# Optimization experiments

Measured on AMD Instinct MI355X. Metric: run time of the kernel, lower is better.

Reference implementation:

```python
import jax, jax.numpy as jnp
from jax import lax
import numpy as np

B, T, D_IN, H, EPS = 32, 256, 256, 1024, 1e-5


def setup_inputs() -> dict:
    key = jax.random.key(0)
    ks = jax.random.split(key, 9)
    s = lambda fan_in: 1.0 / np.sqrt(fan_in)
    merged0, merged1 = D_IN + H, H + H
    series = jax.random.normal(ks[0], (B, T, D_IN), dtype=jnp.float32)
    # Fused gate weights: columns are [in_gate | forget | candidate | out] (4 Linears concatenated)
    W0 = jax.random.uniform(ks[1], (merged0, 4 * H), jnp.float32, -s(merged0), s(merged0))
    b0 = jax.random.uniform(ks[2], (4 * H,), jnp.float32, -s(merged0), s(merged0))
    g0 = jnp.ones((H,), jnp.float32)
    beta0 = jnp.zeros((H,), jnp.float32)
    W1 = jax.random.uniform(ks[3], (merged1, 4 * H), jnp.float32, -s(merged1), s(merged1))
    b1 = jax.random.uniform(ks[4], (4 * H,), jnp.float32, -s(merged1), s(merged1))
    g1 = jnp.ones((H,), jnp.float32)
    beta1 = jnp.zeros((H,), jnp.float32)
    return {"series": series, "W0": W0, "b0": b0, "g0": g0, "beta0": beta0,
            "W1": W1, "b1": b1, "g1": g1, "beta1": beta1}


def _layer_norm(x, g, beta):
    mu = jnp.mean(x, axis=-1, keepdims=True)
    var = jnp.mean((x - mu) ** 2, axis=-1, keepdims=True)
    return (x - mu) * lax.rsqrt(var + EPS) * g + beta


def _run_layer(x_seq, W, b, g, beta):
    # x_seq: [B, T, D]; exp-gated LSTM cell scanned over time
    batch = x_seq.shape[0]

    def step(carry, x_t):
        h, c = carry
        merged = jnp.concatenate([x_t, h], axis=-1)          # [B, D+H]
        z = merged @ W + b                                    # [B, 4H] fused 4 projections
        zi, zf, zc, zo = jnp.split(z, 4, axis=-1)
        in_gate = jnp.exp(jnp.clip(zi, -6.0, 3.0))
        forget_gate = jnp.exp(jnp.clip(zf, -6.0, 3.0))
        candidate = jnp.tanh(zc)
        c_next = forget_gate * c + in_gate * candidate
        h_next = jax.nn.sigmoid(zo) * jnp.tanh(_layer_norm(c_next, g, beta))
        return (h_next, c_next), h_next

    h0 = jnp.zeros((batch, H), x_seq.dtype)
    c0 = jnp.zeros((batch, H), x_seq.dtype)
    _, hs = lax.scan(step, (h0, c0), jnp.swapaxes(x_seq, 0, 1))  # hs: [T, B, H]
    return jnp.swapaxes(hs, 0, 1)


def reference(series, W0, b0, g0, beta0, W1, b1, g1, beta1):
    out = _run_layer(series, W0, b0, g0, beta0)
    # dropout p=0.0 -> identity between layers
    out = _run_layer(out, W1, b1, g1, beta1)
    return out[:, -1, :]
```

## Files before the change

### kernel.cpp

```cpp
#include <hip/hip_runtime.h>
#include <hip/hip_bf16.h>
#include <cstddef>

typedef __bf16 bf16_t;
typedef _Float16 f16_t;
typedef bf16_t bf16x8 __attribute__((ext_vector_type(8)));
typedef bf16_t bf16x4 __attribute__((ext_vector_type(4)));
typedef f16_t  f16x8  __attribute__((ext_vector_type(8)));
typedef float  f32x4  __attribute__((ext_vector_type(4)));
typedef unsigned u32x4 __attribute__((ext_vector_type(4)));
typedef unsigned u32x2 __attribute__((ext_vector_type(2)));

#define T_STEPS 256
#define BATCH   32
#define HDIM    1024
#define ZDIM    4096

constexpr size_t SZ_HSEQ  = (size_t)8192 * 1024 * 2;
constexpr size_t SZ_HBUF  = (size_t)2 * 32 * 512 * 4;
constexpr size_t SZ_SP    = (size_t)2 * 4 * 8 * 128 * 4;
constexpr size_t SZ_HST   = (size_t)32 * 1024 * 2;
constexpr size_t SZ_CST   = (size_t)32 * 1024 * 4;
constexpr size_t SZ_MU    = 256;
constexpr size_t SZ_TAIL  = SZ_HBUF + SZ_SP + 2*SZ_HST + SZ_CST + SZ_MU;
constexpr int    FILL_WORDS = (int)((SZ_HBUF + SZ_SP) / 4);

constexpr int SLAB_STRIDE = 264;
constexpr int HL_STRIDE   = 1040;
constexpr int SCAN_LDS    = 2 * 64 * SLAB_STRIDE * 2;

__global__ void init_fill(unsigned* __restrict__ p, int n) {
    int i = blockIdx.x * blockDim.x + threadIdx.x;
    if (i < n) p[i] = 0xFFFFFFFFu;
}

__device__ __forceinline__ void split_bf16(float v, bf16_t& hi, bf16_t& lo) {
    hi = (bf16_t)v;
    lo = (bf16_t)(v - (float)hi);
}
__device__ __forceinline__ unsigned short f16_bits(f16_t f) {
    union { unsigned short u; f16_t f2; } x; x.f2 = f; return x.u;
}
__device__ __forceinline__ float tanh_fast(float x) {
    float e = __expf(2.f * x);
    return 1.f - 2.f * __builtin_amdgcn_rcpf(e + 1.f);
}
__device__ __forceinline__ void bar_lds() {
    asm volatile("s_waitcnt lgkmcnt(0)" ::: "memory");
    __builtin_amdgcn_s_barrier();
    asm volatile("" ::: "memory");
}

template<int KTOT, int MODE>
__global__ __launch_bounds__(256) void gemm_xp(
    const float*  __restrict__ Afp,
    const bf16_t* __restrict__ Ahi,
    const bf16_t* __restrict__ Alo,
    const float*  __restrict__ W,
    const float*  __restrict__ bias,
    float*        __restrict__ xp,
    int t0)
{
    __shared__ bf16_t Ash[64][40], Asl[64][40], Bsh[64][40], Bsl[64][40];
    const int bm = blockIdx.x / (ZDIM/64);
    const int bn = blockIdx.x % (ZDIM/64);
    const int tid  = threadIdx.x;
    const int lane = tid & 63;
    const int w    = tid >> 6;
    const int wm = w >> 1, wn = w & 1;
    const int q   = lane >> 4;
    const int l15 = lane & 15;

    f32x4 acc[2][2] = {};

    const int sm = tid & 63;
    const int sk = (tid >> 6) * 8;
    const int gr = t0*32 + bm*64 + sm;
    const float*  Arow  = nullptr;
    const bf16_t* Ahrow = nullptr;
    const bf16_t* Alrow = nullptr;
    if constexpr (MODE == 0) {
        int tt = gr >> 5, bb = gr & 31;
        Arow = Afp + ((size_t)bb * T_STEPS + tt) * 256;
    } else {
        Ahrow = Ahi + (size_t)gr * HDIM;
        Alrow = Alo + (size_t)gr * HDIM;
    }
    const int gcol = bn*64 + sm;

    for (int k0 = 0; k0 < KTOT; k0 += 32) {
        if constexpr (MODE == 0) {
            f32x4 a0 = *(const f32x4*)(Arow + k0 + sk);
            f32x4 a1 = *(const f32x4*)(Arow + k0 + sk + 4);
            #pragma unroll
            for (int j = 0; j < 4; ++j) {
                split_bf16(a0[j], Ash[sm][sk+j],   Asl[sm][sk+j]);
                split_bf16(a1[j], Ash[sm][sk+4+j], Asl[sm][sk+4+j]);
            }
        } else {
            *(bf16x8*)&Ash[sm][sk] = *(const bf16x8*)(Ahrow + k0 + sk);
            *(bf16x8*)&Asl[sm][sk] = *(const bf16x8*)(Alrow + k0 + sk);
        }
        #pragma unroll
        for (int j = 0; j < 8; ++j) {
            float wv = W[(size_t)(k0 + sk + j) * ZDIM + gcol];
            split_bf16(wv, Bsh[sm][sk+j], Bsl[sm][sk+j]);
        }
        __syncthreads();
        #pragma unroll
        for (int mt = 0; mt < 2; ++mt) {
            #pragma unroll
            for (int nt = 0; nt < 2; ++nt) {
                bf16x8 ah = *(const bf16x8*)&Ash[wm*32 + mt*16 + l15][q*8];
                bf16x8 al = *(const bf16x8*)&Asl[wm*32 + mt*16 + l15][q*8];
                bf16x8 bh = *(const bf16x8*)&Bsh[wn*32 + nt*16 + l15][q*8];
                bf16x8 bl = *(const bf16x8*)&Bsl[wn*32 + nt*16 + l15][q*8];
                acc[mt][nt] = __builtin_amdgcn_mfma_f32_16x16x32_bf16(ah, bh, acc[mt][nt], 0, 0, 0);
                acc[mt][nt] = __builtin_amdgcn_mfma_f32_16x16x32_bf16(al, bh, acc[mt][nt], 0, 0, 0);
                acc[mt][nt] = __builtin_amdgcn_mfma_f32_16x16x32_bf16(ah, bl, acc[mt][nt], 0, 0, 0);
            }
        }
        __syncthreads();
    }
    #pragma unroll
    for (int mt = 0; mt < 2; ++mt) {
        int row = bm*64 + wm*32 + mt*16 + q*4;
        #pragma unroll
        for (int nt = 0; nt < 2; ++nt) {
            int col = bn*64 + wn*32 + nt*16 + l15;
            float bia = bias[col];
            #pragma unroll
            for (int r = 0; r < 4; ++r)
                xp[(size_t)(row + r)*ZDIM + col] = acc[mt][nt][r] + bia;
        }
    }
}

__global__ __launch_bounds__(256, 1) void scan_kernel(
    const float* __restrict__ Wh,
    const float* __restrict__ xp,
    const float* __restrict__ gamma,
    const float* __restrict__ beta,
    unsigned*    Hbuf,
    unsigned*    Sp,
    bf16_t*      __restrict__ hseq_hi,
    bf16_t*      __restrict__ hseq_lo,
    float*       __restrict__ outlast,
    bf16_t*      __restrict__ hst_hi,
    bf16_t*      __restrict__ hst_lo,
    float*       __restrict__ cstate,
    float*       __restrict__ mustate,
    int t0, int t1)
{
    extern __shared__ char smem[];
    f16_t* slab_hi = (f16_t*)smem;
    f16_t* slab_lo = (f16_t*)(smem + 64*SLAB_STRIDE*2);
    f16_t* hl      = (f16_t*)smem;
    float* swred   = (float*)(smem + 8*HL_STRIDE*2);
    float* sredS   = swred + 64;

    const int gid = blockIdx.x >> 6;
    const int lid = blockIdx.x & 63;
    const int B0  = gid * 8;
    const int H0  = lid * 16;
    const int tid  = threadIdx.x;
    const int lane = tid & 63;
    const int w    = tid >> 6;
    const int q    = lane >> 4;
    const int l15  = lane & 15;

    f16x8 wf_hi[32], wf_lo[32];
    {
        const int kw   = tid >> 6;
        const int strip= (tid >> 4) & 3;
        const int col  = tid & 15;
        const int gc2  = strip*1024 + H0 + col;
        const int rr_w = col*4 + strip;
        #pragma unroll
        for (int s = 0; s < 4; ++s) {
            for (int j = 0; j < 64; ++j) {
                int kk = j*4 + kw;
                float v = Wh[(size_t)(s*256 + kk)*ZDIM + gc2];
                f16_t hi = (f16_t)v;
                f16_t lo = (f16_t)((v - (float)hi) * 2048.f);
                slab_hi[rr_w*SLAB_STRIDE + kk] = hi;
                slab_lo[rr_w*SLAB_STRIDE + kk] = lo;
            }
            __syncthreads();
            #pragma unroll
            for (int kbl = 0; kbl < 8; ++kbl) {
                wf_hi[s*8+kbl] = *(const f16x8*)&slab_hi[(16*w + l15)*SLAB_STRIDE + kbl*32 + q*8];
                wf_lo[s*8+kbl] = *(const f16x8*)&slab_lo[(16*w + l15)*SLAB_STRIDE + kbl*32 + q*8];
            }
            __syncthreads();
        }
    }

    const int  bidx  = l15;
    const bool valid = bidx < 8;
    const int  batch = B0 + bidx;
    const int  hcl   = 4*w + q;
    const int  hcg   = H0 + hcl;
    const size_t xpbase = (size_t)batch * ZDIM + (size_t)H0 + hcl;
    const int hrow  = (l15 < 8) ? l15 : 7;

    const int half   = lane >> 5;
    const int lane32 = lane & 31;
    const int rr     = 2*w + half;
    const int rbatch = B0 + rr;

    float g_own = 0.f, b_own = 0.f;
    if (valid) { g_own = gamma[hcg]; b_own = beta[hcg]; }

    float c = 0.f, mu_own = 0.f;
    if (t0 > 0) {
        if (valid) {
            c = cstate[(size_t)batch*HDIM + hcg];
            mu_own = mustate[batch];
        }
        const int cb = tid * 4;
        #pragma unroll
        for (int r = 0; r < 8; ++r) {
            bf16x4 vh = *(const bf16x4*)&hst_hi[(size_t)(B0+r)*HDIM + cb];
            bf16x4 vl = *(const bf16x4*)&hst_lo[(size_t)(B0+r)*HDIM + cb];
            #pragma unroll
            for (int e = 0; e < 4; ++e)
                hl[r*HL_STRIDE + cb + e] = (f16_t)((float)vh[e] + (float)vl[e]);
        }
    }
    __syncthreads();

    float xpv[4] = {0.f, 0.f, 0.f, 0.f};
    if (valid) {
        const float* xpt = xp + xpbase;
        #pragma unroll
        for (int r = 0; r < 4; ++r) xpv[r] = xpt[(size_t)r * 1024];
    }

    const bool is_l0 = (hseq_hi != nullptr);

    #pragma unroll 1
    for (int t = t0; t < t1; ++t) {
        f32x4 acc_hh = {0.f,0.f,0.f,0.f}, acc_lh = acc_hh;
        if (t > 0) {
            const f16_t* Bp = hl + (size_t)hrow * HL_STRIDE + q*8;
            #pragma unroll
            for (int kb = 0; kb < 32; ++kb) {
                f16x8 b = *(const f16x8*)(Bp + kb*32);
                acc_hh = __builtin_amdgcn_mfma_f32_16x16x32_f16(wf_hi[kb], b, acc_hh, 0, 0, 0);
                acc_lh = __builtin_amdgcn_mfma_f32_16x16x32_f16(wf_lo[kb], b, acc_lh, 0, 0, 0);
            }
        }
        float z[4];
        #pragma unroll
        for (int r = 0; r < 4; ++r)
            z[r] = (acc_hh[r] + acc_lh[r]*(1.f/2048.f)) + xpv[r];

        float zi = fminf(fmaxf(z[0], -6.f), 3.f);
        float zf = fminf(fmaxf(z[1], -6.f), 3.f);
        float ig = __expf(zi);
        float fg = __expf(zf);
        float cand = tanh_fast(z[2]);
        float sg = 1.f / (1.f + __expf(-z[3]));
        c = fg * c + ig * cand;

        const int par = t & 1;
        const unsigned tg = (unsigned)(t & 3);
        const unsigned tgpat = (unsigned)(t & 1) | (((unsigned)(t >> 1) & 1u) << 16);

        float dm = valid ? (c - mu_own) : 0.f;
        float s1 = dm, s2 = dm*dm;
        s1 += __shfl_xor(s1, 16); s2 += __shfl_xor(s2, 16);
        s1 += __shfl_xor(s1, 32); s2 += __shfl_xor(s2, 32);
        if (lane < 8) { swred[(w*8+lane)*2] = s1; swred[(w*8+lane)*2+1] = s2; }
        bar_lds();

        if (tid < 8) {
            float S1p = swred[tid*2]       + swred[(8+tid)*2]
                      + swred[(16+tid)*2]  + swred[(24+tid)*2];
            float S2p = swred[tid*2+1]     + swred[(8+tid)*2+1]
                      + swred[(16+tid)*2+1]+ swred[(24+tid)*2+1];
            u32x2 pk;
            pk[0] = (__float_as_uint(S1p) & ~3u) | tg;
            pk[1] = (__float_as_uint(S2p) & ~3u) | tg;
            *(volatile u32x2*)(Sp + (((size_t)par*4 + gid)*8 + tid)*128 + (size_t)lid*2) = pk;
        }

        if (valid && t+1 < t1) {
            const float* xpt = xp + (size_t)(t+1 - t0) * (BATCH*ZDIM) + xpbase;
            #pragma unroll
            for (int r = 0; r < 4; ++r) xpv[r] = xpt[(size_t)r * 1024];
        }

        {
            const int prr = tid >> 5, jj = tid & 31;
            volatile const u32x4* spb =
                (volatile const u32x4*)(Sp + (((size_t)par*4 + gid)*8 + prr)*128 + (size_t)jj*4);
            u32x4 sv = *spb;
            while ((((sv[0]^tg)|(sv[1]^tg)|(sv[2]^tg)|(sv[3]^tg)) & 3u) != 0u) {
                __builtin_amdgcn_s_sleep(1);
                sv = *spb;
            }
            float s1p = __uint_as_float(sv[0] & ~3u) + __uint_as_float(sv[2] & ~3u);
            float s2p = __uint_as_float(sv[1] & ~3u) + __uint_as_float(sv[3] & ~3u);
            #pragma unroll
            for (int m = 1; m < 32; m <<= 1) {
                s1p += __shfl_xor(s1p, m);
                s2p += __shfl_xor(s2p, m);
            }
            if (jj == 0) { sredS[prr*2] = s1p; sredS[prr*2+1] = s2p; }
        }
        bar_lds();

        const bool carry = (t == t1-1) && (t1 < T_STEPS);
        unsigned hbs = 0;
        if (valid) {
            float S1 = sredS[bidx*2], S2 = sredS[bidx*2+1];
            float dmu = S1 * (1.f/1024.f);
            float mu  = mu_own + dmu;
            float var = S2 * (1.f/1024.f) - dmu*dmu;
            float rsig = rsqrtf(var + 1e-5f);
            mu_own = mu;
            float ln   = (c - mu) * rsig * g_own + b_own;
            float hval = sg * tanh_fast(ln);
            if (is_l0) {
                bf16_t hi, lo; split_bf16(hval, hi, lo);
                hseq_hi[((size_t)t*32 + batch)*HDIM + hcg] = hi;
                hseq_lo[((size_t)t*32 + batch)*HDIM + hcg] = lo;
            }
            if (carry) {
                bf16_t hi, lo; split_bf16(hval, hi, lo);
                hst_hi[(size_t)batch*HDIM + hcg] = hi;
                hst_lo[(size_t)batch*HDIM + hcg] = lo;
            }
            if (outlast && t == T_STEPS-1)
                outlast[(size_t)batch*HDIM + hcg] = hval;
            unsigned tb = (q & 1) ? ((unsigned)(t >> 1) & 1u) : ((unsigned)t & 1u);
            hbs = ((unsigned)f16_bits((f16_t)hval) & 0xFFFEu) | tb;
        }
        unsigned pb2 = __shfl_xor(hbs, 16);
        if (valid && !(q & 1)) {
            unsigned dw = hbs | (pb2 << 16);
            *(volatile unsigned*)(Hbuf + ((size_t)par*32 + batch)*512 + ((unsigned)hcg >> 1)) = dw;
        }

        volatile const u32x4* hb4 =
            (volatile const u32x4*)(Hbuf + ((size_t)par*32 + rbatch)*512) + lane32;
        u32x4 pv[4];
        #pragma unroll
        for (int k = 0; k < 4; ++k) pv[k] = hb4[(size_t)k*32];
        for (;;) {
            bool bad = false;
            #pragma unroll
            for (int k = 0; k < 4; ++k) {
                unsigned m = ((pv[k][0]^tgpat)|(pv[k][1]^tgpat)
                             |(pv[k][2]^tgpat)|(pv[k][3]^tgpat)) & 0x00010001u;
                if (m) { pv[k] = hb4[(size_t)k*32]; bad = true; }
            }
            if (!bad) break;
            __builtin_amdgcn_s_sleep(1);
        }
        #pragma unroll
        for (int k = 0; k < 4; ++k) {
            u32x4 vv = pv[k] & 0xFFFEFFFEu;
            *(u32x4*)&hl[(size_t)rr*HL_STRIDE + (size_t)k*256 + (size_t)lane32*8] = vv;
        }
        bar_lds();
    }

    if (t1 < T_STEPS) {
        if (valid) cstate[(size_t)batch*HDIM + hcg] = c;
        if (lid == 0 && w == 0 && q == 0 && valid) mustate[batch] = mu_own;
    }
}

extern "C" void kernel_launch(void* const* d_in, const int* in_sizes, int n_in,
                              void* d_out, int out_size, void* d_ws, size_t ws_size,
                              hipStream_t stream) {
    (void)in_sizes; (void)n_in;
    const float* series = (const float*)d_in[0];
    const float* W0  = (const float*)d_in[1];
    const float* b0  = (const float*)d_in[2];
    const float* g0  = (const float*)d_in[3];
    const float* be0 = (const float*)d_in[4];
    const float* W1  = (const float*)d_in[5];
    const float* b1  = (const float*)d_in[6];
    const float* g1  = (const float*)d_in[7];
    const float* be1 = (const float*)d_in[8];
    float* out = (float*)d_out;
    unsigned char* ws = (unsigned char*)d_ws;

    int cT = 0;
    const int cands[4] = {256, 128, 64, 32};
    for (int i = 0; i < 4; ++i) {
        size_t need = (size_t)cands[i]*32*ZDIM*4 + 2*SZ_HSEQ + SZ_TAIL;
        if (need <= ws_size) { cT = cands[i]; break; }
    }
    if (cT == 0) {
        (void)hipMemsetAsync(d_out, 0, (size_t)out_size * sizeof(float), stream);
        return;
    }
    const size_t sz_xp = (size_t)cT*32*ZDIM*4;
    unsigned char* p = ws;
    float*    xp      = (float*)p;    p += sz_xp;
    bf16_t*   hseq_hi = (bf16_t*)p;   p += SZ_HSEQ;
    bf16_t*   hseq_lo = (bf16_t*)p;   p += SZ_HSEQ;
    unsigned* Hbuf    = (unsigned*)p; p += SZ_HBUF;
    unsigned* Sp      = (unsigned*)p; p += SZ_SP;
    bf16_t*   hst_hi  = (bf16_t*)p;   p += SZ_HST;
    bf16_t*   hst_lo  = (bf16_t*)p;   p += SZ_HST;
    float*    cstate  = (float*)p;    p += SZ_CST;
    float*    mustate = (float*)p;

    (void)hipFuncSetAttribute((const void*)scan_kernel,
                              hipFuncAttributeMaxDynamicSharedMemorySize, SCAN_LDS);

    const int nch = T_STEPS / cT;
    const int gemm_grid = (cT*32/64) * (ZDIM/64);

    init_fill<<<(FILL_WORDS + 255)/256, 256, 0, stream>>>(Hbuf, FILL_WORDS);
    for (int ci = 0; ci < nch; ++ci) {
        int t0 = ci*cT, t1 = t0 + cT;
        gemm_xp<256, 0><<<gemm_grid, 256, 0, stream>>>(
            series, nullptr, nullptr, W0, b0, xp, t0);
        scan_kernel<<<256, 256, SCAN_LDS, stream>>>(
            W0 + (size_t)256*ZDIM, xp, g0, be0, Hbuf, Sp,
            hseq_hi, hseq_lo, nullptr, hst_hi, hst_lo, cstate, mustate, t0, t1);
    }
    init_fill<<<(FILL_WORDS + 255)/256, 256, 0, stream>>>(Hbuf, FILL_WORDS);
    for (int ci = 0; ci < nch; ++ci) {
        int t0 = ci*cT, t1 = t0 + cT;
        gemm_xp<1024, 1><<<gemm_grid, 256, 0, stream>>>(
            nullptr, hseq_hi, hseq_lo, W1, b1, xp, t0);
        scan_kernel<<<256, 256, SCAN_LDS, stream>>>(
            W1 + (size_t)1024*ZDIM, xp, g1, be1, Hbuf, Sp,
            nullptr, nullptr, out, hst_hi, hst_lo, cstate, mustate, t0, t1);
    }
}
```

Baseline: 4.172 ms.

## Merge two scan blocks per workgroup to halve cross-block sync participants

The persistent scan kernel now runs 128 workgroups of 512 threads, each holding two 16-column hidden slices, instead of 256 workgroups of 256 threads. This halves the number of partial layer-norm sums exchanged through global memory and the number of blocks in each spin-wait, and each block now loads only 8 batch rows of h per step. The final step's h exchange is also skipped. The cost is a longer serialized weight preload, more LDS reduction work per block, and fewer blocks spread across the CUs.

```diff
diff --git a/kernel.cpp b/kernel.cpp
--- a/kernel.cpp
+++ b/kernel.cpp
@@ -18,7 +18,7 @@
 
 constexpr size_t SZ_HSEQ  = (size_t)8192 * 1024 * 2;
 constexpr size_t SZ_HBUF  = (size_t)2 * 32 * 512 * 4;
-constexpr size_t SZ_SP    = (size_t)2 * 4 * 8 * 128 * 4;
+constexpr size_t SZ_SP    = (size_t)2 * 4 * 8 * 32 * 8;
 constexpr size_t SZ_HST   = (size_t)32 * 1024 * 2;
 constexpr size_t SZ_CST   = (size_t)32 * 1024 * 4;
 constexpr size_t SZ_MU    = 256;
@@ -136,7 +136,7 @@
     }
 }
 
-__global__ __launch_bounds__(256, 1) void scan_kernel(
+__global__ __launch_bounds__(512, 1) void scan_kernel(
     const float* __restrict__ Wh,
     const float* __restrict__ xp,
     const float* __restrict__ gamma,
@@ -157,57 +157,63 @@
     f16_t* slab_lo = (f16_t*)(smem + 64*SLAB_STRIDE*2);
     f16_t* hl      = (f16_t*)smem;
     float* swred   = (float*)(smem + 8*HL_STRIDE*2);
-    float* sredS   = swred + 64;
-
-    const int gid = blockIdx.x >> 6;
-    const int lid = blockIdx.x & 63;
+    float* sredS   = swred + 128;
+
+    const int gid = blockIdx.x >> 5;
+    const int sub = blockIdx.x & 31;
     const int B0  = gid * 8;
-    const int H0  = lid * 16;
     const int tid  = threadIdx.x;
     const int lane = tid & 63;
     const int w    = tid >> 6;
+    const int wl   = w & 3;
+    const int vb   = w >> 2;
+    const int vlid = sub*2 + vb;
+    const int H0   = vlid * 16;
     const int q    = lane >> 4;
     const int l15  = lane & 15;
 
     f16x8 wf_hi[32], wf_lo[32];
     {
-        const int kw   = tid >> 6;
+        const int col  = tid & 15;
         const int strip= (tid >> 4) & 3;
-        const int col  = tid & 15;
-        const int gc2  = strip*1024 + H0 + col;
+        const int kw   = (tid >> 6) & 3;
+        const int rep  = tid >> 8;
         const int rr_w = col*4 + strip;
-        #pragma unroll
-        for (int s = 0; s < 4; ++s) {
-            for (int j = 0; j < 64; ++j) {
-                int kk = j*4 + kw;
-                float v = Wh[(size_t)(s*256 + kk)*ZDIM + gc2];
-                f16_t hi = (f16_t)v;
-                f16_t lo = (f16_t)((v - (float)hi) * 2048.f);
-                slab_hi[rr_w*SLAB_STRIDE + kk] = hi;
-                slab_lo[rr_w*SLAB_STRIDE + kk] = lo;
-            }
-            __syncthreads();
-            #pragma unroll
-            for (int kbl = 0; kbl < 8; ++kbl) {
-                wf_hi[s*8+kbl] = *(const f16x8*)&slab_hi[(16*w + l15)*SLAB_STRIDE + kbl*32 + q*8];
-                wf_lo[s*8+kbl] = *(const f16x8*)&slab_lo[(16*w + l15)*SLAB_STRIDE + kbl*32 + q*8];
-            }
-            __syncthreads();
+        for (int p = 0; p < 2; ++p) {
+            const int gc2 = strip*1024 + (sub*2 + p)*16 + col;
+            #pragma unroll 1
+            for (int s = 0; s < 4; ++s) {
+                for (int jj = 0; jj < 32; ++jj) {
+                    int kk = (rep*32 + jj)*4 + kw;
+                    float v = Wh[(size_t)(s*256 + kk)*ZDIM + gc2];
+                    f16_t hi = (f16_t)v;
+                    f16_t lo = (f16_t)((v - (float)hi) * 2048.f);
+                    slab_hi[rr_w*SLAB_STRIDE + kk] = hi;
+                    slab_lo[rr_w*SLAB_STRIDE + kk] = lo;
+                }
+                __syncthreads();
+                if (vb == p) {
+                    #pragma unroll
+                    for (int kbl = 0; kbl < 8; ++kbl) {
+                        wf_hi[s*8+kbl] = *(const f16x8*)&slab_hi[(16*wl + l15)*SLAB_STRIDE + kbl*32 + q*8];
+                        wf_lo[s*8+kbl] = *(const f16x8*)&slab_lo[(16*wl + l15)*SLAB_STRIDE + kbl*32 + q*8];
+                    }
+                }
+                __syncthreads();
+            }
         }
     }
 
     const int  bidx  = l15;
     const bool valid = bidx < 8;
     const int  batch = B0 + bidx;
-    const int  hcl   = 4*w + q;
+    const int  hcl   = 4*wl + q;
     const int  hcg   = H0 + hcl;
     const size_t xpbase = (size_t)batch * ZDIM + (size_t)H0 + hcl;
     const int hrow  = (l15 < 8) ? l15 : 7;
 
-    const int half   = lane >> 5;
-    const int lane32 = lane & 31;
-    const int rr     = 2*w + half;
-    const int rbatch = B0 + rr;
+    const int rr   = tid >> 6;
+    const int rof  = (tid & 63) * 8;
 
     float g_own = 0.f, b_own = 0.f;
     if (valid) { g_own = gamma[hcg]; b_own = beta[hcg]; }
@@ -218,14 +224,16 @@
             c = cstate[(size_t)batch*HDIM + hcg];
             mu_own = mustate[batch];
         }
-        const int cb = tid * 4;
-        #pragma unroll
-        for (int r = 0; r < 8; ++r) {
-            bf16x4 vh = *(const bf16x4*)&hst_hi[(size_t)(B0+r)*HDIM + cb];
-            bf16x4 vl = *(const bf16x4*)&hst_lo[(size_t)(B0+r)*HDIM + cb];
-            #pragma unroll
-            for (int e = 0; e < 4; ++e)
-                hl[r*HL_STRIDE + cb + e] = (f16_t)((float)vh[e] + (float)vl[e]);
+        if (tid < 256) {
+            const int cb = tid * 4;
+            #pragma unroll
+            for (int r = 0; r < 8; ++r) {
+                bf16x4 vh = *(const bf16x4*)&hst_hi[(size_t)(B0+r)*HDIM + cb];
+                bf16x4 vl = *(const bf16x4*)&hst_lo[(size_t)(B0+r)*HDIM + cb];
+                #pragma unroll
+                for (int e = 0; e < 4; ++e)
+                    hl[r*HL_STRIDE + cb + e] = (f16_t)((float)vh[e] + (float)vl[e]);
+            }
         }
     }
     __syncthreads();
@@ -276,14 +284,16 @@
         bar_lds();
 
         if (tid < 8) {
-            float S1p = swred[tid*2]       + swred[(8+tid)*2]
-                      + swred[(16+tid)*2]  + swred[(24+tid)*2];
-            float S2p = swred[tid*2+1]     + swred[(8+tid)*2+1]
-                      + swred[(16+tid)*2+1]+ swred[(24+tid)*2+1];
+            float S1p = 0.f, S2p = 0.f;
+            #pragma unroll
+            for (int ww = 0; ww < 8; ++ww) {
+                S1p += swred[(ww*8+tid)*2];
+                S2p += swred[(ww*8+tid)*2+1];
+            }
             u32x2 pk;
             pk[0] = (__float_as_uint(S1p) & ~3u) | tg;
             pk[1] = (__float_as_uint(S2p) & ~3u) | tg;
-            *(volatile u32x2*)(Sp + (((size_t)par*4 + gid)*8 + tid)*128 + (size_t)lid*2) = pk;
+            *(volatile u32x2*)(Sp + ((((size_t)par*4 + gid)*8 + tid)*32 + sub)*2) = pk;
         }
 
         if (valid && t+1 < t1) {
@@ -292,23 +302,23 @@
             for (int r = 0; r < 4; ++r) xpv[r] = xpt[(size_t)r * 1024];
         }
 
-        {
-            const int prr = tid >> 5, jj = tid & 31;
-            volatile const u32x4* spb =
-                (volatile const u32x4*)(Sp + (((size_t)par*4 + gid)*8 + prr)*128 + (size_t)jj*4);
-            u32x4 sv = *spb;
-            while ((((sv[0]^tg)|(sv[1]^tg)|(sv[2]^tg)|(sv[3]^tg)) & 3u) != 0u) {
+        if (tid < 256) {
+            const int pbt = tid >> 5, bb = tid & 31;
+            volatile const u32x2* spb =
+                (volatile const u32x2*)(Sp + ((((size_t)par*4 + gid)*8 + pbt)*32 + bb)*2);
+            u32x2 sv = *spb;
+            while (((sv[0]^tg)|(sv[1]^tg)) & 3u) {
                 __builtin_amdgcn_s_sleep(1);
                 sv = *spb;
             }
-            float s1p = __uint_as_float(sv[0] & ~3u) + __uint_as_float(sv[2] & ~3u);
-            float s2p = __uint_as_float(sv[1] & ~3u) + __uint_as_float(sv[3] & ~3u);
+            float s1p = __uint_as_float(sv[0] & ~3u);
+            float s2p = __uint_as_float(sv[1] & ~3u);
             #pragma unroll
             for (int m = 1; m < 32; m <<= 1) {
                 s1p += __shfl_xor(s1p, m);
                 s2p += __shfl_xor(s2p, m);
             }
-            if (jj == 0) { sredS[prr*2] = s1p; sredS[prr*2+1] = s2p; }
+            if (bb == 0) { sredS[pbt*2] = s1p; sredS[pbt*2+1] = s2p; }
         }
         bar_lds();
 
@@ -344,33 +354,34 @@
             *(volatile unsigned*)(Hbuf + ((size_t)par*32 + batch)*512 + ((unsigned)hcg >> 1)) = dw;
         }
 
-        volatile const u32x4* hb4 =
-            (volatile const u32x4*)(Hbuf + ((size_t)par*32 + rbatch)*512) + lane32;
-        u32x4 pv[4];
-        #pragma unroll
-        for (int k = 0; k < 4; ++k) pv[k] = hb4[(size_t)k*32];
-        for (;;) {
-            bool bad = false;
-            #pragma unroll
-            for (int k = 0; k < 4; ++k) {
-                unsigned m = ((pv[k][0]^tgpat)|(pv[k][1]^tgpat)
-                             |(pv[k][2]^tgpat)|(pv[k][3]^tgpat)) & 0x00010001u;
-                if (m) { pv[k] = hb4[(size_t)k*32]; bad = true; }
-            }
-            if (!bad) break;
-            __builtin_amdgcn_s_sleep(1);
-        }
-        #pragma unroll
-        for (int k = 0; k < 4; ++k) {
-            u32x4 vv = pv[k] & 0xFFFEFFFEu;
-            *(u32x4*)&hl[(size_t)rr*HL_STRIDE + (size_t)k*256 + (size_t)lane32*8] = vv;
-        }
-        bar_lds();
+        if (t + 1 < t1) {
+            volatile const u32x4* hb4 =
+                (volatile const u32x4*)(Hbuf + ((size_t)par*32 + B0 + rr)*512 + rof);
+            u32x4 pv[2];
+            pv[0] = hb4[0]; pv[1] = hb4[1];
+            for (;;) {
+                bool bad = false;
+                #pragma unroll
+                for (int k = 0; k < 2; ++k) {
+                    unsigned m = ((pv[k][0]^tgpat)|(pv[k][1]^tgpat)
+                                 |(pv[k][2]^tgpat)|(pv[k][3]^tgpat)) & 0x00010001u;
+                    if (m) { pv[k] = hb4[k]; bad = true; }
+                }
+                if (!bad) break;
+                __builtin_amdgcn_s_sleep(1);
+            }
+            #pragma unroll
+            for (int k = 0; k < 2; ++k) {
+                u32x4 vv = pv[k] & 0xFFFEFFFEu;
+                *(u32x4*)&hl[(size_t)rr*HL_STRIDE + (size_t)(rof + k*4)*2] = vv;
+            }
+            bar_lds();
+        }
     }
 
     if (t1 < T_STEPS) {
         if (valid) cstate[(size_t)batch*HDIM + hcg] = c;
-        if (lid == 0 && w == 0 && q == 0 && valid) mustate[batch] = mu_own;
+        if (sub == 0 && vb == 0 && wl == 0 && q == 0 && valid) mustate[batch] = mu_own;
     }
 }
 
@@ -423,7 +434,7 @@
         int t0 = ci*cT, t1 = t0 + cT;
         gemm_xp<256, 0><<<gemm_grid, 256, 0, stream>>>(
             series, nullptr, nullptr, W0, b0, xp, t0);
-        scan_kernel<<<256, 256, SCAN_LDS, stream>>>(
+        scan_kernel<<<128, 512, SCAN_LDS, stream>>>(
             W0 + (size_t)256*ZDIM, xp, g0, be0, Hbuf, Sp,
             hseq_hi, hseq_lo, nullptr, hst_hi, hst_lo, cstate, mustate, t0, t1);
     }
@@ -432,7 +443,7 @@
         int t0 = ci*cT, t1 = t0 + cT;
         gemm_xp<1024, 1><<<gemm_grid, 256, 0, stream>>>(
             nullptr, hseq_hi, hseq_lo, W1, b1, xp, t0);
-        scan_kernel<<<256, 256, SCAN_LDS, stream>>>(
+        scan_kernel<<<128, 512, SCAN_LDS, stream>>>(
             W1 + (size_t)1024*ZDIM, xp, g1, be1, Hbuf, Sp,
             nullptr, nullptr, out, hst_hi, hst_lo, cstate, mustate, t0, t1);
     }
```

Result: slower. 5.830 ms (+39.7%).

## Split h-state exchange wait into halves overlapped with recurrent MFMA

Applied to the files above, without the earlier changes.

The cross-block spin-wait for the next step's hidden state is split in two. At the end of a step the code waits only for the first half of the K range. The wait for the second half is deferred until after the MFMAs over the first half have been issued in the next step. This hides part of the inter-block synchronization latency behind matrix work. It adds an extra LDS barrier per step, and the mustate store condition changes from w==0&&q==0 to hcl==0, which may or may not be equivalent.

```diff
diff --git a/kernel.cpp b/kernel.cpp
--- a/kernel.cpp
+++ b/kernel.cpp
@@ -239,13 +239,38 @@
 
     const bool is_l0 = (hseq_hi != nullptr);
 
+    bool pend = false;
+    u32x4 pv2 = {0,0,0,0}, pv3 = {0,0,0,0};
+    unsigned tgp = 0;
+    volatile const u32x4* hb4p = nullptr;
+
     #pragma unroll 1
     for (int t = t0; t < t1; ++t) {
         f32x4 acc_hh = {0.f,0.f,0.f,0.f}, acc_lh = acc_hh;
         if (t > 0) {
             const f16_t* Bp = hl + (size_t)hrow * HL_STRIDE + q*8;
             #pragma unroll
-            for (int kb = 0; kb < 32; ++kb) {
+            for (int kb = 0; kb < 16; ++kb) {
+                f16x8 b = *(const f16x8*)(Bp + kb*32);
+                acc_hh = __builtin_amdgcn_mfma_f32_16x16x32_f16(wf_hi[kb], b, acc_hh, 0, 0, 0);
+                acc_lh = __builtin_amdgcn_mfma_f32_16x16x32_f16(wf_lo[kb], b, acc_lh, 0, 0, 0);
+            }
+            if (pend) {
+                for (;;) {
+                    unsigned m = ((pv2[0]^tgp)|(pv2[1]^tgp)|(pv2[2]^tgp)|(pv2[3]^tgp)
+                                 |(pv3[0]^tgp)|(pv3[1]^tgp)|(pv3[2]^tgp)|(pv3[3]^tgp)) & 0x00010001u;
+                    if (!m) break;
+                    pv2 = hb4p[2*32];
+                    pv3 = hb4p[3*32];
+                    __builtin_amdgcn_s_sleep(1);
+                }
+                *(u32x4*)&hl[(size_t)rr*HL_STRIDE + 2*256 + (size_t)lane32*8] = pv2 & 0xFFFEFFFEu;
+                *(u32x4*)&hl[(size_t)rr*HL_STRIDE + 3*256 + (size_t)lane32*8] = pv3 & 0xFFFEFFFEu;
+                bar_lds();
+                pend = false;
+            }
+            #pragma unroll
+            for (int kb = 16; kb < 32; ++kb) {
                 f16x8 b = *(const f16x8*)(Bp + kb*32);
                 acc_hh = __builtin_amdgcn_mfma_f32_16x16x32_f16(wf_hi[kb], b, acc_hh, 0, 0, 0);
                 acc_lh = __builtin_amdgcn_mfma_f32_16x16x32_f16(wf_lo[kb], b, acc_lh, 0, 0, 0);
@@ -344,33 +369,35 @@
             *(volatile unsigned*)(Hbuf + ((size_t)par*32 + batch)*512 + ((unsigned)hcg >> 1)) = dw;
         }
 
-        volatile const u32x4* hb4 =
-            (volatile const u32x4*)(Hbuf + ((size_t)par*32 + rbatch)*512) + lane32;
-        u32x4 pv[4];
-        #pragma unroll
-        for (int k = 0; k < 4; ++k) pv[k] = hb4[(size_t)k*32];
-        for (;;) {
-            bool bad = false;
-            #pragma unroll
-            for (int k = 0; k < 4; ++k) {
-                unsigned m = ((pv[k][0]^tgpat)|(pv[k][1]^tgpat)
-                             |(pv[k][2]^tgpat)|(pv[k][3]^tgpat)) & 0x00010001u;
-                if (m) { pv[k] = hb4[(size_t)k*32]; bad = true; }
-            }
-            if (!bad) break;
-            __builtin_amdgcn_s_sleep(1);
-        }
-        #pragma unroll
-        for (int k = 0; k < 4; ++k) {
-            u32x4 vv = pv[k] & 0xFFFEFFFEu;
-            *(u32x4*)&hl[(size_t)rr*HL_STRIDE + (size_t)k*256 + (size_t)lane32*8] = vv;
-        }
-        bar_lds();
+        if (t + 1 < t1) {
+            volatile const u32x4* hb4 =
+                (volatile const u32x4*)(Hbuf + ((size_t)par*32 + rbatch)*512) + lane32;
+            u32x4 pv0 = hb4[0*32];
+            u32x4 pv1 = hb4[1*32];
+            pv2 = hb4[2*32];
+            pv3 = hb4[3*32];
+            for (;;) {
+                unsigned m = ((pv0[0]^tgpat)|(pv0[1]^tgpat)|(pv0[2]^tgpat)|(pv0[3]^tgpat)
+                             |(pv1[0]^tgpat)|(pv1[1]^tgpat)|(pv1[2]^tgpat)|(pv1[3]^tgpat)) & 0x00010001u;
+                if (!m) break;
+                pv0 = hb4[0*32];
+                pv1 = hb4[1*32];
+                __builtin_amdgcn_s_sleep(1);
+            }
+            *(u32x4*)&hl[(size_t)rr*HL_STRIDE + 0*256 + (size_t)lane32*8] = pv0 & 0xFFFEFFFEu;
+            *(u32x4*)&hl[(size_t)rr*HL_STRIDE + 1*256 + (size_t)lane32*8] = pv1 & 0xFFFEFFFEu;
+            bar_lds();
+            pend = true;
+            tgp  = tgpat;
+            hb4p = hb4;
+        }
     }
 
     if (t1 < T_STEPS) {
-        if (valid) cstate[(size_t)batch*HDIM + hcg] = c;
-        if (lid == 0 && w == 0 && q == 0 && valid) mustate[batch] = mu_own;
+        if (valid) {
+            cstate[(size_t)batch*HDIM + hcg] = c;
+            if (lid == 0 && hcl == 0) mustate[batch] = mu_own;
+        }
     }
 }
 
```

New measurement: 4.216 ms. About the same (+1.0%).

## Enlarge xp GEMM tile to 128 rows and skip final-step h exchange

Applied to the files above, without the earlier changes.

The input-projection GEMM now computes a 128x64 tile per block, with each wave owning 32 rows and all 64 columns. The split-bf16 W tile is reused across twice as many rows and the grid is halved, which cuts the redundant fp32 W loads and bf16 splitting. The scan kernel skips the h broadcast wait and LDS fill on the last step of each chunk, since nothing consumes them. Its spin loops also issue two back-to-back reads per poll. The larger tile raises register use and lowers the block count, which may reduce occupancy.

```diff
diff --git a/kernel.cpp b/kernel.cpp
--- a/kernel.cpp
+++ b/kernel.cpp
@@ -61,45 +61,53 @@
     float*        __restrict__ xp,
     int t0)
 {
-    __shared__ bf16_t Ash[64][40], Asl[64][40], Bsh[64][40], Bsl[64][40];
-    const int bm = blockIdx.x / (ZDIM/64);
-    const int bn = blockIdx.x % (ZDIM/64);
+    __shared__ bf16_t Ash[2][64][40], Asl[2][64][40], Bsh[64][40], Bsl[64][40];
+    const int bm = blockIdx.x >> 6;
+    const int bn = blockIdx.x & 63;
     const int tid  = threadIdx.x;
     const int lane = tid & 63;
     const int w    = tid >> 6;
-    const int wm = w >> 1, wn = w & 1;
-    const int q   = lane >> 4;
-    const int l15 = lane & 15;
-
-    f32x4 acc[2][2] = {};
+    const int q    = lane >> 4;
+    const int l15  = lane & 15;
+
+    f32x4 acc[2][4] = {};
 
     const int sm = tid & 63;
     const int sk = (tid >> 6) * 8;
-    const int gr = t0*32 + bm*64 + sm;
-    const float*  Arow  = nullptr;
-    const bf16_t* Ahrow = nullptr;
-    const bf16_t* Alrow = nullptr;
+    const int grb = t0*32 + bm*128;
+    const float*  Arow0 = nullptr; const float* Arow1 = nullptr;
+    const bf16_t *Ah0=nullptr,*Al0=nullptr,*Ah1=nullptr,*Al1=nullptr;
     if constexpr (MODE == 0) {
-        int tt = gr >> 5, bb = gr & 31;
-        Arow = Afp + ((size_t)bb * T_STEPS + tt) * 256;
+        int g0 = grb + sm;       int t0_ = g0 >> 5, b0_ = g0 & 31;
+        int g1 = grb + 64 + sm;  int t1_ = g1 >> 5, b1_ = g1 & 31;
+        Arow0 = Afp + ((size_t)b0_ * T_STEPS + t0_) * 256;
+        Arow1 = Afp + ((size_t)b1_ * T_STEPS + t1_) * 256;
     } else {
-        Ahrow = Ahi + (size_t)gr * HDIM;
-        Alrow = Alo + (size_t)gr * HDIM;
+        Ah0 = Ahi + (size_t)(grb + sm) * HDIM;
+        Al0 = Alo + (size_t)(grb + sm) * HDIM;
+        Ah1 = Ahi + (size_t)(grb + 64 + sm) * HDIM;
+        Al1 = Alo + (size_t)(grb + 64 + sm) * HDIM;
     }
     const int gcol = bn*64 + sm;
 
     for (int k0 = 0; k0 < KTOT; k0 += 32) {
         if constexpr (MODE == 0) {
-            f32x4 a0 = *(const f32x4*)(Arow + k0 + sk);
-            f32x4 a1 = *(const f32x4*)(Arow + k0 + sk + 4);
+            f32x4 a0 = *(const f32x4*)(Arow0 + k0 + sk);
+            f32x4 a1 = *(const f32x4*)(Arow0 + k0 + sk + 4);
+            f32x4 c0 = *(const f32x4*)(Arow1 + k0 + sk);
+            f32x4 c1 = *(const f32x4*)(Arow1 + k0 + sk + 4);
             #pragma unroll
             for (int j = 0; j < 4; ++j) {
-                split_bf16(a0[j], Ash[sm][sk+j],   Asl[sm][sk+j]);
-                split_bf16(a1[j], Ash[sm][sk+4+j], Asl[sm][sk+4+j]);
+                split_bf16(a0[j], Ash[0][sm][sk+j],   Asl[0][sm][sk+j]);
+                split_bf16(a1[j], Ash[0][sm][sk+4+j], Asl[0][sm][sk+4+j]);
+                split_bf16(c0[j], Ash[1][sm][sk+j],   Asl[1][sm][sk+j]);
+                split_bf16(c1[j], Ash[1][sm][sk+4+j], Asl[1][sm][sk+4+j]);
             }
         } else {
-            *(bf16x8*)&Ash[sm][sk] = *(const bf16x8*)(Ahrow + k0 + sk);
-            *(bf16x8*)&Asl[sm][sk] = *(const bf16x8*)(Alrow + k0 + sk);
+            *(bf16x8*)&Ash[0][sm][sk] = *(const bf16x8*)(Ah0 + k0 + sk);
+            *(bf16x8*)&Asl[0][sm][sk] = *(const bf16x8*)(Al0 + k0 + sk);
+            *(bf16x8*)&Ash[1][sm][sk] = *(const bf16x8*)(Ah1 + k0 + sk);
+            *(bf16x8*)&Asl[1][sm][sk] = *(const bf16x8*)(Al1 + k0 + sk);
         }
         #pragma unroll
         for (int j = 0; j < 8; ++j) {
@@ -109,12 +117,14 @@
         __syncthreads();
         #pragma unroll
         for (int mt = 0; mt < 2; ++mt) {
-            #pragma unroll
-            for (int nt = 0; nt < 2; ++nt) {
-                bf16x8 ah = *(const bf16x8*)&Ash[wm*32 + mt*16 + l15][q*8];
-                bf16x8 al = *(const bf16x8*)&Asl[wm*32 + mt*16 + l15][q*8];
-                bf16x8 bh = *(const bf16x8*)&Bsh[wn*32 + nt*16 + l15][q*8];
-                bf16x8 bl = *(const bf16x8*)&Bsl[wn*32 + nt*16 + l15][q*8];
+            const int half = w >> 1;
+            const int rif  = (w & 1)*32 + mt*16 + l15;
+            bf16x8 ah = *(const bf16x8*)&Ash[half][rif][q*8];
+            bf16x8 al = *(const bf16x8*)&Asl[half][rif][q*8];
+            #pragma unroll
+            for (int nt = 0; nt < 4; ++nt) {
+                bf16x8 bh = *(const bf16x8*)&Bsh[nt*16 + l15][q*8];
+                bf16x8 bl = *(const bf16x8*)&Bsl[nt*16 + l15][q*8];
                 acc[mt][nt] = __builtin_amdgcn_mfma_f32_16x16x32_bf16(ah, bh, acc[mt][nt], 0, 0, 0);
                 acc[mt][nt] = __builtin_amdgcn_mfma_f32_16x16x32_bf16(al, bh, acc[mt][nt], 0, 0, 0);
                 acc[mt][nt] = __builtin_amdgcn_mfma_f32_16x16x32_bf16(ah, bl, acc[mt][nt], 0, 0, 0);
@@ -124,10 +134,10 @@
     }
     #pragma unroll
     for (int mt = 0; mt < 2; ++mt) {
-        int row = bm*64 + wm*32 + mt*16 + q*4;
-        #pragma unroll
-        for (int nt = 0; nt < 2; ++nt) {
-            int col = bn*64 + wn*32 + nt*16 + l15;
+        int row = bm*128 + w*32 + mt*16 + q*4;
+        #pragma unroll
+        for (int nt = 0; nt < 4; ++nt) {
+            int col = bn*64 + nt*16 + l15;
             float bia = bias[col];
             #pragma unroll
             for (int r = 0; r < 4; ++r)
@@ -298,8 +308,12 @@
                 (volatile const u32x4*)(Sp + (((size_t)par*4 + gid)*8 + prr)*128 + (size_t)jj*4);
             u32x4 sv = *spb;
             while ((((sv[0]^tg)|(sv[1]^tg)|(sv[2]^tg)|(sv[3]^tg)) & 3u) != 0u) {
+                u32x4 a = *spb;
+                u32x4 b = *spb;
+                unsigned ma = ((a[0]^tg)|(a[1]^tg)|(a[2]^tg)|(a[3]^tg)) & 3u;
+                sv = ma ? b : a;
+                if (!(((sv[0]^tg)|(sv[1]^tg)|(sv[2]^tg)|(sv[3]^tg)) & 3u)) break;
                 __builtin_amdgcn_s_sleep(1);
-                sv = *spb;
             }
             float s1p = __uint_as_float(sv[0] & ~3u) + __uint_as_float(sv[2] & ~3u);
             float s2p = __uint_as_float(sv[1] & ~3u) + __uint_as_float(sv[3] & ~3u);
@@ -344,33 +358,46 @@
             *(volatile unsigned*)(Hbuf + ((size_t)par*32 + batch)*512 + ((unsigned)hcg >> 1)) = dw;
         }
 
-        volatile const u32x4* hb4 =
-            (volatile const u32x4*)(Hbuf + ((size_t)par*32 + rbatch)*512) + lane32;
-        u32x4 pv[4];
-        #pragma unroll
-        for (int k = 0; k < 4; ++k) pv[k] = hb4[(size_t)k*32];
-        for (;;) {
-            bool bad = false;
+        if (t + 1 < t1) {
+            volatile const u32x4* hb4 =
+                (volatile const u32x4*)(Hbuf + ((size_t)par*32 + rbatch)*512) + lane32;
+            u32x4 pv[4];
+            #pragma unroll
+            for (int k = 0; k < 4; ++k) pv[k] = hb4[(size_t)k*32];
+            for (;;) {
+                bool bad = false;
+                #pragma unroll
+                for (int k = 0; k < 4; ++k) {
+                    unsigned m = ((pv[k][0]^tgpat)|(pv[k][1]^tgpat)
+                                 |(pv[k][2]^tgpat)|(pv[k][3]^tgpat)) & 0x00010001u;
+                    if (m) {
+                        u32x4 a = hb4[(size_t)k*32];
+                        u32x4 b = hb4[(size_t)k*32];
+                        unsigned ma = ((a[0]^tgpat)|(a[1]^tgpat)
+                                      |(a[2]^tgpat)|(a[3]^tgpat)) & 0x00010001u;
+                        pv[k] = ma ? b : a;
+                        unsigned mk = ((pv[k][0]^tgpat)|(pv[k][1]^tgpat)
+                                      |(pv[k][2]^tgpat)|(pv[k][3]^tgpat)) & 0x00010001u;
+                        bad |= (mk != 0u);
+                    }
+                }
+                if (!bad) break;
+                __builtin_amdgcn_s_sleep(1);
+            }
             #pragma unroll
             for (int k = 0; k < 4; ++k) {
-                unsigned m = ((pv[k][0]^tgpat)|(pv[k][1]^tgpat)
-                             |(pv[k][2]^tgpat)|(pv[k][3]^tgpat)) & 0x00010001u;
-                if (m) { pv[k] = hb4[(size_t)k*32]; bad = true; }
-            }
-            if (!bad) break;
-            __builtin_amdgcn_s_sleep(1);
-        }
-        #pragma unroll
-        for (int k = 0; k < 4; ++k) {
-            u32x4 vv = pv[k] & 0xFFFEFFFEu;
-            *(u32x4*)&hl[(size_t)rr*HL_STRIDE + (size_t)k*256 + (size_t)lane32*8] = vv;
-        }
-        bar_lds();
+                u32x4 vv = pv[k] & 0xFFFEFFFEu;
+                *(u32x4*)&hl[(size_t)rr*HL_STRIDE + (size_t)k*256 + (size_t)lane32*8] = vv;
+            }
+            bar_lds();
+        }
     }
 
     if (t1 < T_STEPS) {
-        if (valid) cstate[(size_t)batch*HDIM + hcg] = c;
-        if (lid == 0 && w == 0 && q == 0 && valid) mustate[batch] = mu_own;
+        if (valid) {
+            cstate[(size_t)batch*HDIM + hcg] = c;
+            if (lid == 0 && hcl == 0) mustate[batch] = mu_own;
+        }
     }
 }
 
@@ -416,7 +443,7 @@
                               hipFuncAttributeMaxDynamicSharedMemorySize, SCAN_LDS);
 
     const int nch = T_STEPS / cT;
-    const int gemm_grid = (cT*32/64) * (ZDIM/64);
+    const int gemm_grid = (cT*32/128) * (ZDIM/64);
 
     init_fill<<<(FILL_WORDS + 255)/256, 256, 0, stream>>>(Hbuf, FILL_WORDS);
     for (int ci = 0; ci < nch; ++ci) {
```

Result: slower. 4.510 ms (+8.1%).
